# Optimization experiments

Measured on AMD Instinct MI355X. Metric: run time of the kernel, lower is better.

Reference implementation:

```python
import jax, jax.numpy as jnp
import numpy as np

B, S, D = 4, 4096, 1024
GROUP = 256
HEAD = 128
INNER = 2048


def setup_inputs() -> dict:
    key = jax.random.key(0)
    ks = jax.random.split(key, 16)
    s = 0.02
    return {
        'x': jax.random.normal(ks[0], (B, S, D), jnp.float32),
        'Wv': jax.random.normal(ks[1], (D, INNER), jnp.float32) * s,
        'bv': jnp.zeros((INNER,), jnp.float32),
        'Wg': jax.random.normal(ks[2], (D, INNER), jnp.float32) * s,
        'bg': jnp.zeros((INNER,), jnp.float32),
        'Win': jax.random.normal(ks[3], (D, HEAD), jnp.float32) * s,
        'bin_': jnp.zeros((HEAD,), jnp.float32),
        'Wout': jax.random.normal(ks[4], (INNER, D), jnp.float32) * s,
        'bout': jnp.zeros((D,), jnp.float32),
        'g_qq': 1.0 + jax.random.normal(ks[5], (HEAD,), jnp.float32) * s,
        'b_qq': jnp.zeros((HEAD,), jnp.float32),
        'g_qk': 1.0 + jax.random.normal(ks[6], (HEAD,), jnp.float32) * s,
        'b_qk': jnp.zeros((HEAD,), jnp.float32),
        'g_lq': 1.0 + jax.random.normal(ks[7], (HEAD,), jnp.float32) * s,
        'b_lq': jnp.zeros((HEAD,), jnp.float32),
        'g_lk': 1.0 + jax.random.normal(ks[8], (HEAD,), jnp.float32) * s,
        'b_lk': jnp.zeros((HEAD,), jnp.float32),
    }


def reference(x, Wv, bv, Wg, bg, Win, bin_, Wout, bout,
              g_qq, b_qq, g_qk, b_qk, g_lq, b_lq, g_lk, b_lk):
    b, s, d = x.shape
    g = s // GROUP
    xc = x.reshape(b, g, GROUP, d)                       # [B,G,C,D]
    v = jax.nn.silu(xc @ Wv + bv)                        # [B,G,C,E]
    gate = jax.nn.silu(xc @ Wg + bg)                     # [B,G,C,E]
    x_ = jax.nn.silu(xc @ Win + bin_)                    # [B,G,C,H]
    quad_q = x_ * g_qq + b_qq
    quad_k = x_ * g_qk + b_qk
    lin_q = x_ * g_lq + b_lq
    lin_k = x_ * g_lk + b_lk
    # local quadratic relu^2 attention per chunk
    scale = jnp.asarray(INNER ** 0.5, x.dtype)           # v.size(-1)**0.5
    attn = jnp.einsum('bgns,bgms->bgnm', quad_q, quad_k) / scale
    causal_mask = jnp.triu(jnp.ones((GROUP, GROUP), bool), 1)
    attn = jnp.where(causal_mask, 0.0, attn)
    attn = jnp.square(jax.nn.relu(attn))
    v_quad = jnp.einsum('bgnm,bgme->bgne', attn, v)
    # global causal linear attention: exclusive cumsum of per-chunk k^T v over chunks
    kv = jnp.einsum('bgcs,bgce->bgse', lin_k, v)         # [B,G,H,E]
    kv = jnp.cumsum(kv, axis=1) - kv                     # exclusive over chunk dim
    v_lin = jnp.einsum('bgcs,bgse->bgce', lin_q, kv)
    o = (v_quad + v_lin) * gate
    o = o @ Wout + bout
    return o.reshape(b, s, d)
```

## Files before the change

### kernel.cpp

```cpp
#include <hip/hip_runtime.h>

typedef __attribute__((ext_vector_type(8))) short short8;
typedef __attribute__((ext_vector_type(4))) float floatx4;
typedef __attribute__((ext_vector_type(4))) unsigned short ushort4v;
typedef unsigned short u16;

#define DEV __device__ __forceinline__

DEV u16 f2bf(float f) {
  unsigned int u = __float_as_uint(f);
  u += 0x7fffu + ((u >> 16) & 1u);
  return (u16)(u >> 16);
}
DEV float bf2f(u16 h) { return __uint_as_float(((unsigned int)h) << 16); }
DEV float silu_f(float x) { return x / (1.f + __expf(-x)); }
DEV floatx4 fzero() { floatx4 z = {0.f, 0.f, 0.f, 0.f}; return z; }
DEV floatx4 mfma16(short8 a, short8 b, floatx4 c) {
  return __builtin_amdgcn_mfma_f32_16x16x32_bf16(a, b, c, 0, 0, 0);
}
DEV void gll16(const void* g, void* l) {
  __builtin_amdgcn_global_load_lds((__attribute__((address_space(1))) void*)g,
                                   (__attribute__((address_space(3))) void*)l,
                                   16, 0, 0);
}

__global__ __launch_bounds__(256) void cast_x_kernel(const float* __restrict__ x,
                                                     u16* __restrict__ xb, int n4) {
  int i = blockIdx.x * 256 + threadIdx.x;
  if (i >= n4) return;
  float4 v = ((const float4*)x)[i];
  ushort4v o;
  o[0] = f2bf(v.x); o[1] = f2bf(v.y); o[2] = f2bf(v.z); o[3] = f2bf(v.w);
  *(ushort4v*)&xb[(size_t)i * 4] = o;
}

__global__ __launch_bounds__(256) void transpose_cast_kernel(const float* __restrict__ W,
                                                             u16* __restrict__ WT,
                                                             int K, int N) {
  __shared__ u16 tile[32][36];
  int n0 = blockIdx.x * 32, k0 = blockIdx.y * 32;
  int t = threadIdx.x;
  int r = t >> 3, cs = (t & 7) * 4;
  float4 v = *(const float4*)&W[(size_t)(k0 + r) * N + n0 + cs];
  tile[r][cs + 0] = f2bf(v.x);
  tile[r][cs + 1] = f2bf(v.y);
  tile[r][cs + 2] = f2bf(v.z);
  tile[r][cs + 3] = f2bf(v.w);
  __syncthreads();
  ushort4v o;
  o[0] = tile[cs + 0][r];
  o[1] = tile[cs + 1][r];
  o[2] = tile[cs + 2][r];
  o[3] = tile[cs + 3][r];
  *(ushort4v*)&WT[(size_t)(n0 + r) * K + k0 + cs] = o;
}

DEV void wave_transposed_store(u16* __restrict__ Ct, long chunk_stride,
                               const u16* trw, int chunk, int cbase, int nbase,
                               int lane) {
#pragma unroll
  for (int it = 0; it < 8; ++it) {
    int e_l = it * 8 + (lane >> 3);
    int c_off = (lane & 7) * 8;
    short8 val = *(const short8*)&trw[e_l * 72 + c_off];
    *(short8*)&Ct[(size_t)chunk * chunk_stride + (size_t)(nbase + e_l) * 256 + cbase +
                  c_off] = val;
  }
}


#define PH2(SA, SB, VML, STG, HH)                                            \
  {                                                                          \
    asm volatile("s_waitcnt vmcnt(" #VML ")" ::: "memory");                  \
    if (STG) { STAGE(HH); STAGE((HH) + 1); }                                 \
    _Pragma("unroll") for (int mi_ = 0; mi_ < 8; ++mi_)                      \
        af[mi_] = *(const short8*)&lds[((SA) * 1024 + aoff + mi_ * 64) * 8]; \
    _Pragma("unroll") for (int ni_ = 0; ni_ < 4; ++ni_)                      \
        bf[ni_] = *(const short8*)&lds[((SB) * 1024 + boff + ni_ * 64) * 8]; \
    asm volatile("" ::: "memory");                                           \
    __builtin_amdgcn_s_setprio(1);                                           \
    _Pragma("unroll") for (int mi_ = 0; mi_ < 8; ++mi_)                      \
      _Pragma("unroll") for (int ni_ = 0; ni_ < 4; ++ni_)                    \
          acc[mi_][ni_] = mfma16(af[mi_], bf[ni_], acc[mi_][ni_]);           \
    __builtin_amdgcn_s_setprio(0);                                           \
    asm volatile("" ::: "memory");                                           \
    __builtin_amdgcn_s_barrier();                                            \
    asm volatile("" ::: "memory");                                           \
  }

template <int MODE>
__global__ __launch_bounds__(512, 2) void gemm8(
    const u16* __restrict__ A, const u16* __restrict__ Bt,
    const float* __restrict__ bias0, const float* __restrict__ bias1,
    u16* __restrict__ vT, u16* __restrict__ gate, float* __restrict__ Cf) {
  constexpr int KK = (MODE == 0) ? 1024 : 2048;
  constexpr int NN = (MODE == 0) ? 4096 : 1024;
  constexpr int NT = KK / 64;
  constexpr int NSH = (MODE == 0) ? 4 : 2;

  __shared__ u16 lds[8 * 8192];

  const int t = threadIdx.x;
  const int wave = t >> 6, lane = t & 63;
  const int l15 = lane & 15, l16 = lane >> 4;
  const int b = blockIdx.x;
  const int xcd = b & 7, i = b >> 3;
  const int m0 = (xcd * 8 + (i >> NSH)) * 256;
  const int n0 = (i & ((1 << NSH) - 1)) * 256;
  const int wm = wave >> 2, wn = wave & 3;

  const int o0 = wave * 128 + lane;
  const int r0 = o0 >> 2;
  const int p0 = (o0 & 3) ^ ((r0 >> 1) & 3);
  const u16* srcA = A + (size_t)(m0 + r0) * KK + p0 * 8;
  const u16* srcB = Bt + (size_t)(n0 + r0) * KK + p0 * 8;

  auto STAGE = [&](int h) {
    const int slot = h & 7;
    const int koff = (h >> 2) * 64 + ((h >> 1) & 1) * 32;
    u16* dst = &lds[slot * 8192 + o0 * 8];
    const u16* s = ((h & 1) ? srcB : srcA) + koff;
    gll16(s, dst);
    gll16(s + 16 * KK, dst + 512);
  };

  const int rA = wm * 128 + l15;
  const int aoff = rA * 4 + (l16 ^ ((rA >> 1) & 3));
  const int rB = wn * 64 + l15;
  const int boff = rB * 4 + (l16 ^ ((rB >> 1) & 3));

  floatx4 acc[8][4];
#pragma unroll
  for (int a = 0; a < 8; ++a)
#pragma unroll
    for (int c = 0; c < 4; ++c) acc[a][c] = fzero();
  short8 af[8], bf[4];

#pragma unroll
  for (int h = 0; h < 6; ++h) STAGE(h);
  asm volatile("s_waitcnt vmcnt(8)" ::: "memory");
  asm volatile("" ::: "memory");
  __builtin_amdgcn_s_barrier();
  asm volatile("" ::: "memory");

  for (int T = 0; T < NT - 2; ++T) {
    const int s0 = (T & 1) * 4;
    PH2(s0, s0 + 1, 4, 1, 4 * T + 6)
    PH2(s0 + 2, s0 + 3, 4, 1, 4 * T + 8)
  }
  {
    const int s0 = ((NT - 2) & 1) * 4;
    PH2(s0, s0 + 1, 4, 1, 4 * (NT - 2) + 6)
    PH2(s0 + 2, s0 + 3, 4, 0, 0)
  }
  {
    const int s0 = ((NT - 1) & 1) * 4;
    PH2(s0, s0 + 1, 0, 0, 0)
    PH2(s0 + 2, s0 + 3, 0, 0, 0)
  }

  if constexpr (MODE == 0) {
    const int chunk = m0 >> 8;
    u16* trw = &lds[wave * (64 * 72)];
    if (n0 < 2048) {
      const int e0 = n0 + wn * 64;
#pragma unroll
      for (int th = 0; th < 2; ++th) {
#pragma unroll
        for (int mi2 = 0; mi2 < 4; ++mi2) {
          const int mi = th * 4 + mi2;
#pragma unroll
          for (int ni = 0; ni < 4; ++ni) {
            const float bc = bias0[e0 + ni * 16 + l15];
            ushort4v pk;
#pragma unroll
            for (int r = 0; r < 4; ++r) pk[r] = f2bf(silu_f(acc[mi][ni][r] + bc));
            *(ushort4v*)&trw[(ni * 16 + l15) * 72 + mi2 * 16 + l16 * 4] = pk;
          }
        }
        wave_transposed_store(vT, 2048L * 256, trw, chunk, wm * 128 + th * 64, e0,
                              lane);
      }
    } else {
      const int c0 = n0 - 2048 + wn * 64;
#pragma unroll
      for (int th = 0; th < 2; ++th) {
#pragma unroll
        for (int mi2 = 0; mi2 < 4; ++mi2) {
          const int mi = th * 4 + mi2;
#pragma unroll
          for (int ni = 0; ni < 4; ++ni) {
            const float bc = bias1[c0 + ni * 16 + l15];
#pragma unroll
            for (int r = 0; r < 4; ++r)
              trw[(mi2 * 16 + l16 * 4 + r) * 72 + ni * 16 + l15] =
                  f2bf(silu_f(acc[mi][ni][r] + bc));
          }
        }
#pragma unroll
        for (int it = 0; it < 8; ++it) {
          const int m_l = it * 8 + (lane >> 3);
          const int n_off = (lane & 7) * 8;
          *(short8*)&gate[(size_t)(m0 + wm * 128 + th * 64 + m_l) * 2048 + c0 +
                          n_off] = *(const short8*)&trw[m_l * 72 + n_off];
        }
      }
    }
  } else {
#pragma unroll
    for (int mi = 0; mi < 8; ++mi)
#pragma unroll
      for (int ni = 0; ni < 4; ++ni) {
        const int col = n0 + wn * 64 + ni * 16 + l15;
        const float bc = bias0[col];
        const int row = m0 + wm * 128 + mi * 16 + l16 * 4;
#pragma unroll
        for (int r = 0; r < 4; ++r)
          Cf[(size_t)(row + r) * NN + col] = acc[mi][ni][r] + bc;
      }
  }
}

template <int MODE>
__global__ __launch_bounds__(256) void gemm_bt(
    const u16* __restrict__ A, const u16* __restrict__ Bt, int M, int N, int K,
    int nshift, const float* __restrict__ bias, u16* __restrict__ Cn,
    float* __restrict__ Cf, u16* __restrict__ Ct, long ct_stride,
    u16* __restrict__ Cn2, u16* __restrict__ Cn3,
    const float* __restrict__ gqq, const float* __restrict__ bqq,
    const float* __restrict__ gqk, const float* __restrict__ bqk,
    const float* __restrict__ glq, const float* __restrict__ blq,
    const float* __restrict__ glk, const float* __restrict__ blk) {
  __shared__ union {
    struct { u16 a[128 * 64]; u16 b[128 * 64]; } st;
    u16 tr[4 * 64 * 72];
  } sm;
  const int t = threadIdx.x;
  const int wave = t >> 6, lane = t & 63;
  const int l15 = lane & 15, l16 = lane >> 4;
  const int ell = blockIdx.x;
  const int xcd = ell & 7, i = ell >> 3;
  const int mtiles_per_xcd = M >> 10;
  const int m0 = (xcd * mtiles_per_xcd + (i >> nshift)) * 128;
  const int n0 = (i & ((1 << nshift) - 1)) * 128;
  const int wm = (wave >> 1) * 64, wn = (wave & 1) * 64;

  floatx4 acc[4][4];
#pragma unroll
  for (int i2 = 0; i2 < 4; ++i2)
#pragma unroll
    for (int j = 0; j < 4; ++j) acc[i2][j] = fzero();

  const u16* pa[4];
  const u16* pb[4];
#pragma unroll
  for (int j = 0; j < 4; ++j) {
    const int c = t + 256 * j;
    const int r = c >> 3, p = c & 7;
    const int g = p ^ (r & 7);
    pa[j] = A + (size_t)(m0 + r) * K + g * 8;
    pb[j] = Bt + (size_t)(n0 + r) * K + g * 8;
  }

  for (int k0 = 0; k0 < K; k0 += 64) {
    __syncthreads();
#pragma unroll
    for (int j = 0; j < 4; ++j) {
      gll16(pa[j] + k0, &sm.st.a[(t + 256 * j) * 8]);
      gll16(pb[j] + k0, &sm.st.b[(t + 256 * j) * 8]);
    }
    __syncthreads();
#pragma unroll
    for (int s = 0; s < 2; ++s) {
      short8 af[4], bfr[4];
#pragma unroll
      for (int mi = 0; mi < 4; ++mi) {
        const int wr = wm + mi * 16 + l15;
        af[mi] = *(const short8*)&sm.st.a[wr * 64 + ((s * 4 + l16) ^ (wr & 7)) * 8];
      }
#pragma unroll
      for (int ni = 0; ni < 4; ++ni) {
        const int wr = wn + ni * 16 + l15;
        bfr[ni] = *(const short8*)&sm.st.b[wr * 64 + ((s * 4 + l16) ^ (wr & 7)) * 8];
      }
#pragma unroll
      for (int mi = 0; mi < 4; ++mi)
#pragma unroll
        for (int ni = 0; ni < 4; ++ni)
          acc[mi][ni] = mfma16(af[mi], bfr[ni], acc[mi][ni]);
    }
  }
  __syncthreads();

  if constexpr (MODE == 3) {
#pragma unroll
    for (int mi = 0; mi < 4; ++mi)
#pragma unroll
      for (int ni = 0; ni < 4; ++ni) {
        const int col = n0 + wn + ni * 16 + l15;
        const float bc = bias[col];
        const int row = m0 + wm + mi * 16 + l16 * 4;
#pragma unroll
        for (int r = 0; r < 4; ++r)
          Cf[(size_t)(row + r) * N + col] = acc[mi][ni][r] + bc;
      }
  } else {
    u16* trw = &sm.tr[wave * 64 * 72];
#pragma unroll
    for (int mi = 0; mi < 4; ++mi)
#pragma unroll
      for (int ni = 0; ni < 4; ++ni) {
        const int col = wn + ni * 16 + l15;
        const float bc = bias[col];
        const float Gqq = gqq[col], Bqq = bqq[col];
        const float Gqk = gqk[col], Bqk = bqk[col];
        const float Glq = glq[col], Blq = blq[col];
        const float Glk = glk[col], Blk = blk[col];
        const int row = m0 + wm + mi * 16 + l16 * 4;
        ushort4v p;
#pragma unroll
        for (int r = 0; r < 4; ++r) {
          const float sv = silu_f(acc[mi][ni][r] + bc);
          const size_t ad = (size_t)(row + r) * N + col;
          Cn[ad] = f2bf(sv * Gqq + Bqq);
          Cn2[ad] = f2bf(sv * Gqk + Bqk);
          Cn3[ad] = f2bf(sv * Glq + Blq);
          p[r] = f2bf(sv * Glk + Blk);
        }
        *(ushort4v*)&trw[(ni * 16 + l15) * 72 + mi * 16 + l16 * 4] = p;
      }
    wave_transposed_store(Ct, ct_stride, trw, (m0 + wm) >> 8, (m0 + wm) & 255, wn,
                          lane);
  }
}

__global__ __launch_bounds__(256) void kv_kernel(const u16* __restrict__ vT,
                                                 const u16* __restrict__ lkT,
                                                 u16* __restrict__ kv) {
  const int chunk = blockIdx.y;
  const int et = blockIdx.x;
  const int w = threadIdx.x >> 6, lane = threadIdx.x & 63;
  const int l15 = lane & 15, l16 = lane >> 4;
  const size_t vb = (size_t)chunk * (2048 * 256) + (size_t)et * (128 * 256);
  const size_t lb = (size_t)chunk * (128 * 256);
  const int we = (w >> 1) * 64, wh = (w & 1) * 64;
  floatx4 acc[4][4];
#pragma unroll
  for (int i = 0; i < 4; ++i)
#pragma unroll
    for (int j = 0; j < 4; ++j) acc[i][j] = fzero();
  for (int kk = 0; kk < 8; ++kk) {
    short8 av[4], bv[4];
#pragma unroll
    for (int mi = 0; mi < 4; ++mi)
      av[mi] = *(const short8*)&vT[vb + (size_t)(we + mi * 16 + l15) * 256 + kk * 32 +
                                   l16 * 8];
#pragma unroll
    for (int ni = 0; ni < 4; ++ni)
      bv[ni] = *(const short8*)&lkT[lb + (size_t)(wh + ni * 16 + l15) * 256 + kk * 32 +
                                    l16 * 8];
#pragma unroll
    for (int mi = 0; mi < 4; ++mi)
#pragma unroll
      for (int ni = 0; ni < 4; ++ni) acc[mi][ni] = mfma16(av[mi], bv[ni], acc[mi][ni]);
  }
  u16* out = kv + (size_t)chunk * (2048 * 128);
#pragma unroll
  for (int mi = 0; mi < 4; ++mi)
#pragma unroll
    for (int ni = 0; ni < 4; ++ni) {
      const int h = wh + ni * 16 + l15;
      const int e = et * 128 + we + mi * 16 + l16 * 4;
#pragma unroll
      for (int r = 0; r < 4; ++r) out[(size_t)(e + r) * 128 + h] = f2bf(acc[mi][ni][r]);
    }
}

__global__ __launch_bounds__(256) void cumsum_kernel(u16* __restrict__ kv) {
  const int idx = blockIdx.x * 256 + threadIdx.x;
  const int b = blockIdx.y;
  float s = 0.f;
  for (int g = 0; g < 16; ++g) {
    const size_t a = (size_t)(b * 16 + g) * 262144 + idx;
    const float v = bf2f(kv[a]);
    kv[a] = f2bf(s);
    s += v;
  }
}

__global__ __launch_bounds__(256) void attn_kernel(
    const u16* __restrict__ qq, const u16* __restrict__ qk, const u16* __restrict__ lq,
    const u16* __restrict__ vT, const u16* __restrict__ kvT,
    u16* __restrict__ gate_op) {
  __shared__ u16 S[64][264];
  const int chunk = blockIdx.y;
  const int e0 = blockIdx.x * 256;
  const int tok0 = chunk * 256;
  const int w = threadIdx.x >> 6, lane = threadIdx.x & 63;
  const int l15 = lane & 15, l16 = lane >> 4;
  const float isc = 0.022097086912079608f;
  const size_t vbase = (size_t)chunk * (2048 * 256);
  const size_t kbase = (size_t)chunk * (2048 * 128);
  const int ew = e0 + w * 64;

  for (int ns = 0; ns < 4; ++ns) {
    const int r0 = ns * 64 + w * 16;
    short8 af[4];
#pragma unroll
    for (int kk = 0; kk < 4; ++kk)
      af[kk] = *(const short8*)&qq[(size_t)(tok0 + r0 + l15) * 128 + kk * 32 + l16 * 8];
    const int mt_cnt = (r0 >> 4) + 1;
    const int mt_all = (ns + 1) * 4;
    const int srow = w * 16 + l16 * 4;
    for (int mt = 0; mt < mt_all; ++mt) {
      if (mt < mt_cnt) {
        floatx4 a = fzero();
#pragma unroll
        for (int kk = 0; kk < 4; ++kk) {
          short8 bq =
              *(const short8*)&qk[(size_t)(tok0 + mt * 16 + l15) * 128 + kk * 32 +
                                  l16 * 8];
          a = mfma16(af[kk], bq, a);
        }
        const int mcol = mt * 16 + l15;
#pragma unroll
        for (int r = 0; r < 4; ++r) {
          const int nrow = r0 + l16 * 4 + r;
          float sv = a[r] * isc;
          sv = (mcol <= nrow) ? sv : 0.f;
          sv = fmaxf(sv, 0.f);
          S[srow + r][mcol] = f2bf(sv * sv);
        }
      } else {
#pragma unroll
        for (int r = 0; r < 4; ++r) S[srow + r][mt * 16 + l15] = (u16)0;
      }
    }
    __syncthreads();

    floatx4 acc[4][4];
#pragma unroll
    for (int i = 0; i < 4; ++i)
#pragma unroll
      for (int j = 0; j < 4; ++j) acc[i][j] = fzero();

    const int ks = (ns + 1) * 2;
    for (int kk = 0; kk < ks; ++kk) {
      short8 sa[4];
#pragma unroll
      for (int nt = 0; nt < 4; ++nt)
        sa[nt] = *(const short8*)&S[nt * 16 + l15][kk * 32 + l16 * 8];
#pragma unroll
      for (int ei = 0; ei < 4; ++ei) {
        short8 vb = *(const short8*)&vT[vbase + (size_t)(ew + ei * 16 + l15) * 256 +
                                        kk * 32 + l16 * 8];
#pragma unroll
        for (int nt = 0; nt < 4; ++nt) acc[nt][ei] = mfma16(sa[nt], vb, acc[nt][ei]);
      }
    }
#pragma unroll
    for (int kk = 0; kk < 4; ++kk) {
      short8 la[4];
#pragma unroll
      for (int nt = 0; nt < 4; ++nt)
        la[nt] = *(const short8*)&lq[(size_t)(tok0 + ns * 64 + nt * 16 + l15) * 128 +
                                     kk * 32 + l16 * 8];
#pragma unroll
      for (int ei = 0; ei < 4; ++ei) {
        short8 kb = *(const short8*)&kvT[kbase + (size_t)(ew + ei * 16 + l15) * 128 +
                                         kk * 32 + l16 * 8];
#pragma unroll
        for (int nt = 0; nt < 4; ++nt) acc[nt][ei] = mfma16(la[nt], kb, acc[nt][ei]);
      }
    }
#pragma unroll
    for (int nt = 0; nt < 4; ++nt)
#pragma unroll
      for (int ei = 0; ei < 4; ++ei) {
        const int e_g = ew + ei * 16 + l15;
        const int nb = tok0 + ns * 64 + nt * 16 + l16 * 4;
#pragma unroll
        for (int r = 0; r < 4; ++r) {
          const size_t ad = (size_t)(nb + r) * 2048 + e_g;
          const float gv = bf2f(gate_op[ad]);
          gate_op[ad] = f2bf(acc[nt][ei][r] * gv);
        }
      }
    __syncthreads();
  }
}

extern "C" void kernel_launch(void* const* d_in, const int* in_sizes, int n_in,
                              void* d_out, int out_size, void* d_ws, size_t ws_size,
                              hipStream_t stream) {
  (void)in_sizes; (void)n_in; (void)out_size; (void)ws_size;
  const float* x = (const float*)d_in[0];
  const float* Wv = (const float*)d_in[1];
  const float* bv = (const float*)d_in[2];
  const float* Wg = (const float*)d_in[3];
  const float* bg = (const float*)d_in[4];
  const float* Win = (const float*)d_in[5];
  const float* bin = (const float*)d_in[6];
  const float* Wout = (const float*)d_in[7];
  const float* bout = (const float*)d_in[8];
  const float* gqq = (const float*)d_in[9];
  const float* bqq = (const float*)d_in[10];
  const float* gqk = (const float*)d_in[11];
  const float* bqk = (const float*)d_in[12];
  const float* glq = (const float*)d_in[13];
  const float* blq = (const float*)d_in[14];
  const float* glk = (const float*)d_in[15];
  const float* blk = (const float*)d_in[16];

  char* p = (char*)d_ws;
  u16* xb = (u16*)p;   p += (size_t)16384 * 1024 * 2;
  u16* wvT = (u16*)p;  p += (size_t)2048 * 1024 * 2;
  u16* wgT = (u16*)p;  p += (size_t)2048 * 1024 * 2;
  u16* winT = (u16*)p; p += (size_t)128 * 1024 * 2;
  u16* woT = (u16*)p;  p += (size_t)1024 * 2048 * 2;
  u16* vTb = (u16*)p;  p += (size_t)64 * 2048 * 256 * 2;
  u16* gate = (u16*)p; p += (size_t)16384 * 2048 * 2;
  u16* qqb = (u16*)p;  p += (size_t)16384 * 128 * 2;
  u16* qkb = (u16*)p;  p += (size_t)16384 * 128 * 2;
  u16* lqb = (u16*)p;  p += (size_t)16384 * 128 * 2;
  u16* lkTb = (u16*)p; p += (size_t)64 * 128 * 256 * 2;
  u16* kvb = (u16*)p;  p += (size_t)64 * 2048 * 128 * 2;

  cast_x_kernel<<<16384, 256, 0, stream>>>(x, xb, 4194304);
  transpose_cast_kernel<<<dim3(64, 32), 256, 0, stream>>>(Wv, wvT, 1024, 2048);
  transpose_cast_kernel<<<dim3(64, 32), 256, 0, stream>>>(Wg, wgT, 1024, 2048);
  transpose_cast_kernel<<<dim3(4, 32), 256, 0, stream>>>(Win, winT, 1024, 128);
  transpose_cast_kernel<<<dim3(32, 64), 256, 0, stream>>>(Wout, woT, 2048, 1024);

  gemm8<0><<<1024, 512, 0, stream>>>(xb, wvT, bv, bg, vTb, gate, nullptr);

  gemm_bt<2><<<128, 256, 0, stream>>>(
      xb, winT, 16384, 128, 1024, 0, bin, qqb, nullptr, lkTb, 128L * 256, qkb, lqb,
      gqq, bqq, gqk, bqk, glq, blq, glk, blk);

  kv_kernel<<<dim3(16, 64), 256, 0, stream>>>(vTb, lkTb, kvb);
  cumsum_kernel<<<dim3(1024, 4), 256, 0, stream>>>(kvb);
  attn_kernel<<<dim3(8, 64), 256, 0, stream>>>(qqb, qkb, lqb, vTb, kvb, gate);

  gemm8<1><<<256, 512, 0, stream>>>(gate, woT, bout, nullptr, nullptr, nullptr,
                                    (float*)d_out);
}
```

Baseline: 555.1 us.

## Double-buffer LDS-to-register fragments to overlap ds_reads with MFMA in gemm8

```diff
diff --git a/kernel.cpp b/kernel.cpp
--- a/kernel.cpp
+++ b/kernel.cpp
@@ -69,23 +69,26 @@
 }
 
 
-#define PH2(SA, SB, VML, STG, HH)                                            \
-  {                                                                          \
-    asm volatile("s_waitcnt vmcnt(" #VML ")" ::: "memory");                  \
-    if (STG) { STAGE(HH); STAGE((HH) + 1); }                                 \
-    _Pragma("unroll") for (int mi_ = 0; mi_ < 8; ++mi_)                      \
-        af[mi_] = *(const short8*)&lds[((SA) * 1024 + aoff + mi_ * 64) * 8]; \
-    _Pragma("unroll") for (int ni_ = 0; ni_ < 4; ++ni_)                      \
-        bf[ni_] = *(const short8*)&lds[((SB) * 1024 + boff + ni_ * 64) * 8]; \
-    asm volatile("" ::: "memory");                                           \
-    __builtin_amdgcn_s_setprio(1);                                           \
-    _Pragma("unroll") for (int mi_ = 0; mi_ < 8; ++mi_)                      \
-      _Pragma("unroll") for (int ni_ = 0; ni_ < 4; ++ni_)                    \
-          acc[mi_][ni_] = mfma16(af[mi_], bf[ni_], acc[mi_][ni_]);           \
-    __builtin_amdgcn_s_setprio(0);                                           \
-    asm volatile("" ::: "memory");                                           \
-    __builtin_amdgcn_s_barrier();                                            \
-    asm volatile("" ::: "memory");                                           \
+#define LOADREGS(LA, LB, SAn, SBn)                                             \
+  _Pragma("unroll") for (int mi_ = 0; mi_ < 8; ++mi_)                          \
+      LA[mi_] = *(const short8*)&lds[((SAn) * 1024 + aoff + mi_ * 64) * 8];    \
+  _Pragma("unroll") for (int ni_ = 0; ni_ < 4; ++ni_)                          \
+      LB[ni_] = *(const short8*)&lds[((SBn) * 1024 + boff + ni_ * 64) * 8];
+
+#define PH5(UA, UB, LA, LB, SAn, SBn, VML, STG, SLA, SLB, KOFF, DORD)          \
+  {                                                                            \
+    asm volatile("s_waitcnt vmcnt(" #VML ")" ::: "memory");                    \
+    if (STG) { STAGE2(SLA, srcA, KOFF); STAGE2(SLB, srcB, KOFF); }             \
+    if (DORD) { LOADREGS(LA, LB, SAn, SBn) }                                   \
+    __builtin_amdgcn_sched_barrier(0);                                         \
+    __builtin_amdgcn_s_setprio(1);                                             \
+    _Pragma("unroll") for (int mi_ = 0; mi_ < 8; ++mi_)                        \
+      _Pragma("unroll") for (int ni_ = 0; ni_ < 4; ++ni_)                      \
+          acc[mi_][ni_] = mfma16(UA[mi_], UB[ni_], acc[mi_][ni_]);             \
+    __builtin_amdgcn_s_setprio(0);                                             \
+    asm volatile("s_waitcnt lgkmcnt(0)" ::: "memory");                         \
+    __builtin_amdgcn_s_barrier();                                              \
+    asm volatile("" ::: "memory");                                             \
   }
 
 template <int MODE>
@@ -115,11 +118,9 @@
   const u16* srcA = A + (size_t)(m0 + r0) * KK + p0 * 8;
   const u16* srcB = Bt + (size_t)(n0 + r0) * KK + p0 * 8;
 
-  auto STAGE = [&](int h) {
-    const int slot = h & 7;
-    const int koff = (h >> 2) * 64 + ((h >> 1) & 1) * 32;
+  auto STAGE2 = [&](int slot, const u16* src, int koff) {
     u16* dst = &lds[slot * 8192 + o0 * 8];
-    const u16* s = ((h & 1) ? srcB : srcA) + koff;
+    const u16* s = src + koff;
     gll16(s, dst);
     gll16(s + 16 * KK, dst + 512);
   };
@@ -134,30 +135,31 @@
   for (int a = 0; a < 8; ++a)
 #pragma unroll
     for (int c = 0; c < 4; ++c) acc[a][c] = fzero();
-  short8 af[8], bf[4];
-
-#pragma unroll
-  for (int h = 0; h < 6; ++h) STAGE(h);
+  short8 afA[8], bfA[4], afB[8], bfB[4];
+
+  STAGE2(0, srcA, 0);  STAGE2(1, srcB, 0);
+  STAGE2(2, srcA, 32); STAGE2(3, srcB, 32);
+  STAGE2(4, srcA, 64); STAGE2(5, srcB, 64);
+  STAGE2(6, srcA, 96); STAGE2(7, srcB, 96);
   asm volatile("s_waitcnt vmcnt(8)" ::: "memory");
-  asm volatile("" ::: "memory");
   __builtin_amdgcn_s_barrier();
   asm volatile("" ::: "memory");
-
-  for (int T = 0; T < NT - 2; ++T) {
-    const int s0 = (T & 1) * 4;
-    PH2(s0, s0 + 1, 4, 1, 4 * T + 6)
-    PH2(s0 + 2, s0 + 3, 4, 1, 4 * T + 8)
-  }
-  {
-    const int s0 = ((NT - 2) & 1) * 4;
-    PH2(s0, s0 + 1, 4, 1, 4 * (NT - 2) + 6)
-    PH2(s0 + 2, s0 + 3, 4, 0, 0)
-  }
-  {
-    const int s0 = ((NT - 1) & 1) * 4;
-    PH2(s0, s0 + 1, 0, 0, 0)
-    PH2(s0 + 2, s0 + 3, 0, 0, 0)
-  }
+  LOADREGS(afA, bfA, 0, 1)
+  asm volatile("s_waitcnt lgkmcnt(0)" ::: "memory");
+  __builtin_amdgcn_s_barrier();
+  asm volatile("" ::: "memory");
+
+#pragma unroll 1
+  for (int TT = 0; TT < (NT - 2) / 2; ++TT) {
+    PH5(afA, bfA, afB, bfB, 2, 3, 4, 1, 0, 1, (2 * TT + 2) * 64, 1)
+    PH5(afB, bfB, afA, bfA, 4, 5, 4, 1, 2, 3, (2 * TT + 2) * 64 + 32, 1)
+    PH5(afA, bfA, afB, bfB, 6, 7, 4, 1, 4, 5, (2 * TT + 3) * 64, 1)
+    PH5(afB, bfB, afA, bfA, 0, 1, 4, 1, 6, 7, (2 * TT + 3) * 64 + 32, 1)
+  }
+  PH5(afA, bfA, afB, bfB, 2, 3, 4, 0, 0, 0, 0, 1)
+  PH5(afB, bfB, afA, bfA, 4, 5, 0, 0, 0, 0, 0, 1)
+  PH5(afA, bfA, afB, bfB, 6, 7, 0, 0, 0, 0, 0, 1)
+  PH5(afB, bfB, afA, bfA, 0, 1, 0, 0, 0, 0, 0, 0)
 
   if constexpr (MODE == 0) {
     const int chunk = m0 >> 8;
```

After: 612.5 us. 10.3% more time.
